# Performance work log

Measured on AMD Instinct MI355X. Metric: run time of the kernel, lower is better.

The kernel has to match this reference:

```python
import jax, jax.numpy as jnp
import numpy as np

H = 8            # heads
SCALE = (512 // H) ** -0.5  # dim_head^-0.5
EPS = 1e-5


def ln(x, w, b):
    mu = jnp.mean(x, axis=-1, keepdims=True)
    var = jnp.var(x, axis=-1, keepdims=True)
    return (x - mu) / jnp.sqrt(var + EPS) * w + b


def attention(x, ctx, wq, wkv, wo, bo):
    # x: [b, i, d], ctx: [b, j, d_ctx]
    b, i, _ = x.shape
    q = x @ wq                       # [b, i, h*dh]
    k, v = jnp.split(ctx @ wkv, 2, axis=-1)
    split_heads = lambda t: t.reshape(t.shape[0], t.shape[1], H, -1).transpose(0, 2, 1, 3)
    q, k, v = split_heads(q), split_heads(k), split_heads(v)
    sim = jnp.einsum('bhid,bhjd->bhij', q, k) * SCALE
    attn = jax.nn.softmax(sim, axis=-1)
    out = jnp.einsum('bhij,bhjd->bhid', attn, v)
    out = out.transpose(0, 2, 1, 3).reshape(b, i, -1)
    return out @ wo + bo


def geglu_ff(x, w1, b1, w2, b2):
    h = x @ w1 + b1
    a, g = jnp.split(h, 2, axis=-1)
    return (a * jax.nn.gelu(g, approximate=False)) @ w2 + b2


def setup_inputs() -> dict:
    key = jax.random.key(0)
    ks = jax.random.split(key, 12)
    D, FF, B, L, N = 512, 2048, 8, 128, 4096
    r = lambda k, s: jax.random.normal(k, s, jnp.float32) * 0.02
    return {
        'context': jax.random.normal(ks[0], (B, N, D), jnp.float32),
        'latents': jax.random.normal(ks[1], (B, L, D), jnp.float32),
        'ca_ln_w': jnp.ones((D,), jnp.float32), 'ca_ln_b': jnp.zeros((D,), jnp.float32),
        'ca_lnc_w': jnp.ones((D,), jnp.float32), 'ca_lnc_b': jnp.zeros((D,), jnp.float32),
        'ca_wq': r(ks[2], (D, D)), 'ca_wkv': r(ks[3], (D, 2 * D)),
        'ca_wo': r(ks[4], (D, D)), 'ca_bo': jnp.zeros((D,), jnp.float32),
        'cf_ln_w': jnp.ones((D,), jnp.float32), 'cf_ln_b': jnp.zeros((D,), jnp.float32),
        'cf_w1': r(ks[5], (D, 2 * FF)), 'cf_b1': jnp.zeros((2 * FF,), jnp.float32),
        'cf_w2': r(ks[6], (FF, D)), 'cf_b2': jnp.zeros((D,), jnp.float32),
        'sa_ln_w': jnp.ones((D,), jnp.float32), 'sa_ln_b': jnp.zeros((D,), jnp.float32),
        'sa_wq': r(ks[7], (D, D)), 'sa_wkv': r(ks[8], (D, 2 * D)),
        'sa_wo': r(ks[9], (D, D)), 'sa_bo': jnp.zeros((D,), jnp.float32),
        'lf_ln_w': jnp.ones((D,), jnp.float32), 'lf_ln_b': jnp.zeros((D,), jnp.float32),
        'lf_w1': r(ks[10], (D, 2 * FF)), 'lf_b1': jnp.zeros((2 * FF,), jnp.float32),
        'lf_w2': r(ks[11], (FF, D)), 'lf_b2': jnp.zeros((D,), jnp.float32),
    }


def reference(context, latents,
              ca_ln_w, ca_ln_b, ca_lnc_w, ca_lnc_b, ca_wq, ca_wkv, ca_wo, ca_bo,
              cf_ln_w, cf_ln_b, cf_w1, cf_b1, cf_w2, cf_b2,
              sa_ln_w, sa_ln_b, sa_wq, sa_wkv, sa_wo, sa_bo,
              lf_ln_w, lf_ln_b, lf_w1, lf_b1, lf_w2, lf_b2):
    x = latents
    # PreNorm cross-attention (with context LayerNorm) + residual
    xn = ln(x, ca_ln_w, ca_ln_b)
    cn = ln(context, ca_lnc_w, ca_lnc_b)
    x = attention(xn, cn, ca_wq, ca_wkv, ca_wo, ca_bo) + x
    # PreNorm cross FFN (GEGLU) + residual
    x = geglu_ff(ln(x, cf_ln_w, cf_ln_b), cf_w1, cf_b1, cf_w2, cf_b2) + x
    # PreNorm latent self-attention + residual
    xn = ln(x, sa_ln_w, sa_ln_b)
    x = attention(xn, xn, sa_wq, sa_wkv, sa_wo, sa_bo) + x
    # PreNorm latent FFN (GEGLU) + residual
    x = geglu_ff(ln(x, lf_ln_w, lf_ln_b), lf_w1, lf_b1, lf_w2, lf_b2) + x
    return x
```

## Files before the change

kernel.cpp:

```cpp
#include <hip/hip_runtime.h>
#include <hip/hip_bf16.h>
#include <math.h>


typedef __attribute__((ext_vector_type(8))) short bf16x8;
typedef __attribute__((ext_vector_type(4))) float f32x4;
typedef long i64;
typedef __attribute__((ext_vector_type(2))) long i64x2;

#define DEVI __device__ __forceinline__

DEVI void load_lds16(const void* g, void* l) {
  __builtin_amdgcn_global_load_lds(
      (const __attribute__((address_space(1))) void*)g,
      (__attribute__((address_space(3))) void*)l, 16, 0, 0);
}

DEVI short bfbits(float x) {
  __hip_bfloat16 h = __float2bfloat16(x);
  return *reinterpret_cast<short*>(&h);
}

DEVI unsigned int fp8pk2(float a, float b) {
  return __builtin_amdgcn_cvt_pk_fp8_f32(a, b, 0, false) & 0xffff;
}

DEVI unsigned char fp8b(float x) {
  return (unsigned char)(__builtin_amdgcn_cvt_pk_fp8_f32(x, x, 0, false) & 0xff);
}

__global__ __launch_bounds__(256, 4) void gemm_sk(
    const __hip_bfloat16* __restrict__ A, const __hip_bfloat16* __restrict__ Bt,
    float* __restrict__ P, int M, int N, int K) {
  const int nwg = gridDim.x * gridDim.y;
  const int lid = blockIdx.y * gridDim.x + blockIdx.x;
  const int work = (lid & 7) * (nwg >> 3) + (lid >> 3);
  const int n0 = (work % gridDim.x) * 128;
  const int m0 = (work / gridDim.x) * 128;
  const int KS = K / gridDim.z;
  const int kbeg = blockIdx.z * KS;

  const int t = threadIdx.x;
  const int w = t >> 6, l = t & 63;
  const int lr = l & 15, lk = l >> 4;
  const int wm = (w >> 1) * 64, wn = (w & 1) * 64;
  __shared__ __hip_bfloat16 Al[2][128 * 32];
  __shared__ __hip_bfloat16 Bl[2][128 * 32];

  f32x4 acc[4][4];
  const f32x4 z = {0.f, 0.f, 0.f, 0.f};
#pragma unroll
  for (int i = 0; i < 4; ++i)
#pragma unroll
    for (int j = 0; j < 4; ++j) acc[i][j] = z;

  const int srow = w * 16 + (l >> 2);
  const int scol = ((l & 3) ^ ((l >> 3) & 3)) * 8;
  const __hip_bfloat16* Ag = A + (size_t)(m0 + srow) * K + kbeg + scol;
  const __hip_bfloat16* Bg = Bt + (size_t)(n0 + srow) * K + kbeg + scol;

#define STAGE(buf, k0)                                                   \
  {                                                                      \
    load_lds16(Ag + (k0), (char*)Al[buf] + w * 1024);                    \
    load_lds16(Ag + (size_t)64 * K + (k0), (char*)Al[buf] + 4096 + w * 1024); \
    load_lds16(Bg + (k0), (char*)Bl[buf] + w * 1024);                    \
    load_lds16(Bg + (size_t)64 * K + (k0), (char*)Bl[buf] + 4096 + w * 1024); \
  }

  STAGE(0, 0);
  __syncthreads();
  int cur = 0;
  const int rs = (lk ^ ((lr >> 1) & 3)) * 16;
  for (int k0 = 0; k0 < KS; k0 += 32) {
    if (k0 + 32 < KS) STAGE(cur ^ 1, k0 + 32);
    bf16x8 af[4], bfr[4];
#pragma unroll
    for (int i = 0; i < 4; ++i)
      af[i] = *(const bf16x8*)((const char*)Al[cur] + ((wm + i * 16 + lr) * 64 + rs));
#pragma unroll
    for (int j = 0; j < 4; ++j)
      bfr[j] = *(const bf16x8*)((const char*)Bl[cur] + ((wn + j * 16 + lr) * 64 + rs));
#pragma unroll
    for (int i = 0; i < 4; ++i)
#pragma unroll
      for (int j = 0; j < 4; ++j)
        acc[i][j] = __builtin_amdgcn_mfma_f32_16x16x32_bf16(af[i], bfr[j], acc[i][j], 0, 0, 0);
    __syncthreads();
    cur ^= 1;
  }
#undef STAGE

  float* Pz = P + (size_t)blockIdx.z * M * N;
#pragma unroll
  for (int i = 0; i < 4; ++i) {
    const int row = m0 + wm + i * 16 + lk * 4;
#pragma unroll
    for (int j = 0; j < 4; ++j) {
      const int col = n0 + wn + j * 16 + lr;
#pragma unroll
      for (int r = 0; r < 4; ++r)
        Pz[(size_t)(row + r) * N + col] = acc[i][j][r];
    }
  }
}

__global__ __launch_bounds__(256) void reduce_sk(
    const float* __restrict__ P, const float* __restrict__ bias,
    const float* __restrict__ res, float* __restrict__ out, int SK) {
  const int i = (blockIdx.x * 256 + threadIdx.x) * 4;
  f32x4 v = *(const f32x4*)&bias[i & 511];
  const f32x4 rr = *(const f32x4*)&res[i];
  v += rr;
  for (int s = 0; s < SK; ++s) v += *(const f32x4*)&P[(size_t)s * 524288 + i];
  *(f32x4*)&out[i] = v;
}

__global__ __launch_bounds__(256) void reduce_ln_sk(
    const float* __restrict__ P, const float* __restrict__ bias,
    const float* __restrict__ res, float* __restrict__ xout,
    const float* __restrict__ w, const float* __restrict__ b,
    __hip_bfloat16* __restrict__ y, int SK) {
  const int row = blockIdx.x * 4 + (threadIdx.x >> 6);
  const int l = threadIdx.x & 63;
  const size_t base = (size_t)row * 512 + l * 8;
  f32x4 v0 = *(const f32x4*)&res[base];
  f32x4 v1 = *(const f32x4*)&res[base + 4];
  v0 += *(const f32x4*)&bias[l * 8];
  v1 += *(const f32x4*)&bias[l * 8 + 4];
  for (int s = 0; s < SK; ++s) {
    v0 += *(const f32x4*)&P[(size_t)s * 524288 + base];
    v1 += *(const f32x4*)&P[(size_t)s * 524288 + base + 4];
  }
  *(f32x4*)&xout[base] = v0;
  *(f32x4*)&xout[base + 4] = v1;
  float s1 = 0.f, s2 = 0.f;
#pragma unroll
  for (int e = 0; e < 4; ++e) {
    s1 += v0[e] + v1[e];
    s2 += v0[e] * v0[e] + v1[e] * v1[e];
  }
#pragma unroll
  for (int d = 1; d < 64; d <<= 1) {
    s1 += __shfl_xor(s1, d);
    s2 += __shfl_xor(s2, d);
  }
  const float mean = s1 * (1.f / 512.f);
  const float var = s2 * (1.f / 512.f) - mean * mean;
  const float rstd = rsqrtf(var + 1e-5f);
  const f32x4 w0 = *(const f32x4*)&w[l * 8], w1 = *(const f32x4*)&w[l * 8 + 4];
  const f32x4 b0 = *(const f32x4*)&b[l * 8], b1 = *(const f32x4*)&b[l * 8 + 4];
  bf16x8 o;
#pragma unroll
  for (int e = 0; e < 4; ++e) {
    o[e] = bfbits((v0[e] - mean) * rstd * w0[e] + b0[e]);
    o[e + 4] = bfbits((v1[e] - mean) * rstd * w1[e] + b1[e]);
  }
  *(bf16x8*)&y[base] = o;
}

__global__ __launch_bounds__(256, 4) void gemm_geglu(
    const __hip_bfloat16* __restrict__ A, const __hip_bfloat16* __restrict__ Bt,
    __hip_bfloat16* __restrict__ Cb, const float* __restrict__ bias) {
  const int K = 512;
  const int nwg = gridDim.x * gridDim.y;
  const int lid = blockIdx.y * gridDim.x + blockIdx.x;
  const int work = (lid & 7) * (nwg >> 3) + (lid >> 3);
  const int n0 = (work % gridDim.x) * 128;
  const int m0 = (work / gridDim.x) * 64;

  const int t = threadIdx.x;
  const int w = t >> 6, l = t & 63;
  const int lr = l & 15, lk = l >> 4;
  const int wm = (w >> 1) * 32, wn = (w & 1) * 64;
  __shared__ __hip_bfloat16 Al[2][64 * 32];
  __shared__ __hip_bfloat16 Bl[2][128 * 32];

  f32x4 acc[2][4];
  const f32x4 z = {0.f, 0.f, 0.f, 0.f};
#pragma unroll
  for (int i = 0; i < 2; ++i)
#pragma unroll
    for (int j = 0; j < 4; ++j) acc[i][j] = z;

  const int srow = w * 16 + (l >> 2);
  const int scol = ((l & 3) ^ ((l >> 3) & 3)) * 8;
  const __hip_bfloat16* Ag = A + (size_t)(m0 + srow) * K + scol;
  const __hip_bfloat16* Bg = Bt + (size_t)(n0 + srow) * K + scol;

#define STAGE(buf, k0)                                                   \
  {                                                                      \
    load_lds16(Ag + (k0), (char*)Al[buf] + w * 1024);                    \
    load_lds16(Bg + (k0), (char*)Bl[buf] + w * 1024);                    \
    load_lds16(Bg + (size_t)64 * K + (k0), (char*)Bl[buf] + 4096 + w * 1024); \
  }

  STAGE(0, 0);
  __syncthreads();
  int cur = 0;
  const int rs = (lk ^ ((lr >> 1) & 3)) * 16;
  for (int k0 = 0; k0 < K; k0 += 32) {
    if (k0 + 32 < K) STAGE(cur ^ 1, k0 + 32);
    bf16x8 af[2], bfr[4];
#pragma unroll
    for (int i = 0; i < 2; ++i)
      af[i] = *(const bf16x8*)((const char*)Al[cur] + ((wm + i * 16 + lr) * 64 + rs));
#pragma unroll
    for (int j = 0; j < 4; ++j)
      bfr[j] = *(const bf16x8*)((const char*)Bl[cur] + ((wn + j * 16 + lr) * 64 + rs));
#pragma unroll
    for (int i = 0; i < 2; ++i)
#pragma unroll
      for (int j = 0; j < 4; ++j)
        acc[i][j] = __builtin_amdgcn_mfma_f32_16x16x32_bf16(af[i], bfr[j], acc[i][j], 0, 0, 0);
    __syncthreads();
    cur ^= 1;
  }
#undef STAGE

  const int nb = (n0 + wn) >> 1;
  float ba[2], bg[2];
#pragma unroll
  for (int jj = 0; jj < 2; ++jj) {
    ba[jj] = bias[nb + jj * 16 + lr];
    bg[jj] = bias[2048 + nb + jj * 16 + lr];
  }
#pragma unroll
  for (int i = 0; i < 2; ++i) {
    const int row = m0 + wm + i * 16 + lk * 4;
#pragma unroll
    for (int jj = 0; jj < 2; ++jj) {
      const int col = nb + jj * 16 + lr;
#pragma unroll
      for (int r = 0; r < 4; ++r) {
        const float a = acc[i][jj][r] + ba[jj];
        const float g = acc[i][jj + 2][r] + bg[jj];
        const float ge = 0.5f * g * (1.f + erff(g * 0.70710678118f));
        Cb[(size_t)(row + r) * 2048 + col] = __float2bfloat16(a * ge);
      }
    }
  }
}

__global__ __launch_bounds__(256, 4) void projx_kernel(
    const unsigned char* __restrict__ ctx8, const unsigned char* __restrict__ wkv8,
    __hip_bfloat16* __restrict__ Kb, __hip_bfloat16* __restrict__ Vt,
    const unsigned char* __restrict__ xq8, const unsigned char* __restrict__ wq8,
    __hip_bfloat16* __restrict__ Qb) {
  const int nwg = gridDim.x;
  const int lid = blockIdx.x;
  const int work = (lid & 7) * (nwg >> 3) + (lid >> 3);

  const unsigned char *A, *Bt;
  int m0, n0, mode;
  if (work < 2048) {
    m0 = (work >> 3) * 128;
    n0 = (work & 7) * 128;
    A = ctx8; Bt = wkv8;
    mode = (n0 < 512) ? 0 : 1;
  } else {
    const int idx = work - 2048;
    m0 = (idx >> 2) * 128;
    n0 = (idx & 3) * 128;
    A = xq8; Bt = wq8;
    mode = 2;
  }

  const int t = threadIdx.x;
  const int w = t >> 6, l = t & 63;
  const int lr = l & 15, lk = l >> 4;
  const int wm = (w >> 1) * 64, wn = (w & 1) * 64;
  __shared__ unsigned char Al[2][128 * 64];
  __shared__ unsigned char Bl[2][128 * 64];

  f32x4 acc[4][4];
  const f32x4 z = {0.f, 0.f, 0.f, 0.f};
#pragma unroll
  for (int i = 0; i < 4; ++i)
#pragma unroll
    for (int j = 0; j < 4; ++j) acc[i][j] = z;

  const int srow = w * 16 + (l >> 2);
  const int sc = ((l & 3) ^ ((l >> 3) & 3)) * 16;
  const unsigned char* Ag = A + (size_t)(m0 + srow) * 512 + sc;
  const unsigned char* Bg = Bt + (size_t)(n0 + srow) * 512 + sc;

#define STAGE(buf, kb)                                                   \
  {                                                                      \
    load_lds16(Ag + (kb), (char*)Al[buf] + w * 1024);                    \
    load_lds16(Ag + (size_t)64 * 512 + (kb), (char*)Al[buf] + 4096 + w * 1024); \
    load_lds16(Bg + (kb), (char*)Bl[buf] + w * 1024);                    \
    load_lds16(Bg + (size_t)64 * 512 + (kb), (char*)Bl[buf] + 4096 + w * 1024); \
  }

  STAGE(0, 0);
  __syncthreads();
  int cur = 0;
  const int rs = (lk ^ ((lr >> 1) & 3)) * 16;
  for (int tt = 0; tt < 8; ++tt) {
    if (tt < 7) STAGE(cur ^ 1, (tt + 1) * 64);
    i64 af[2][4], bfr[2][4];
#pragma unroll
    for (int i = 0; i < 4; ++i) {
      const int ar = wm + i * 16 + lr;
      const i64x2 v = *(const i64x2*)((const char*)Al[cur] + ar * 64 + rs);
      af[0][i] = v[0];
      af[1][i] = v[1];
    }
#pragma unroll
    for (int j = 0; j < 4; ++j) {
      const int br = wn + j * 16 + lr;
      const i64x2 v = *(const i64x2*)((const char*)Bl[cur] + br * 64 + rs);
      bfr[0][j] = v[0];
      bfr[1][j] = v[1];
    }
#pragma unroll
    for (int i = 0; i < 4; ++i)
#pragma unroll
      for (int j = 0; j < 4; ++j) {
        acc[i][j] = __builtin_amdgcn_mfma_f32_16x16x32_fp8_fp8(af[0][i], bfr[0][j], acc[i][j], 0, 0, 0);
        acc[i][j] = __builtin_amdgcn_mfma_f32_16x16x32_fp8_fp8(af[1][i], bfr[1][j], acc[i][j], 0, 0, 0);
      }
    __syncthreads();
    cur ^= 1;
  }
#undef STAGE

  const float SCL = 0.0625f;
  if (mode == 0) {
#pragma unroll
    for (int i = 0; i < 4; ++i) {
      const int row = m0 + wm + i * 16 + lk * 4;
#pragma unroll
      for (int j = 0; j < 4; ++j) {
        const int col = n0 + wn + j * 16 + lr;
#pragma unroll
        for (int r = 0; r < 4; ++r)
          Kb[(size_t)(row + r) * 512 + col] = __float2bfloat16(acc[i][j][r] * SCL);
      }
    }
  } else if (mode == 1) {
#pragma unroll
    for (int i = 0; i < 4; ++i) {
      const int row0 = m0 + wm + i * 16 + lk * 4;
      const int b = row0 >> 12;
      const int key0 = row0 & 4095;
#pragma unroll
      for (int j = 0; j < 4; ++j) {
        const int c = n0 + wn + j * 16 + lr - 512;
        const int hh = c >> 6, dh = c & 63;
        short4 pk;
        pk.x = bfbits(acc[i][j][0] * SCL);
        pk.y = bfbits(acc[i][j][1] * SCL);
        pk.z = bfbits(acc[i][j][2] * SCL);
        pk.w = bfbits(acc[i][j][3] * SCL);
        *(short4*)&Vt[((size_t)((b * 8 + hh) * 64 + dh) << 12) + key0] = pk;
      }
    }
  } else {
#pragma unroll
    for (int i = 0; i < 4; ++i) {
      const int row = m0 + wm + i * 16 + lk * 4;
#pragma unroll
      for (int j = 0; j < 4; ++j) {
        const int col = n0 + wn + j * 16 + lr;
#pragma unroll
        for (int r = 0; r < 4; ++r)
          Qb[(size_t)(row + r) * 512 + col] = __float2bfloat16(acc[i][j][r] * SCL);
      }
    }
  }
}

__global__ __launch_bounds__(256, 4) void proj_kernel(
    const __hip_bfloat16* __restrict__ A, const __hip_bfloat16* __restrict__ Bt,
    __hip_bfloat16* __restrict__ Qb, __hip_bfloat16* __restrict__ Kb,
    __hip_bfloat16* __restrict__ Vt, int qcols, int rpb_shift) {
  const int nwg = gridDim.x * gridDim.y;
  const int lid = blockIdx.y * gridDim.x + blockIdx.x;
  const int work = (lid & 7) * (nwg >> 3) + (lid >> 3);
  const int n0 = (work % gridDim.x) * 128;
  const int m0 = (work / gridDim.x) * 128;
  const int K = 512;

  const int t = threadIdx.x;
  const int w = t >> 6, l = t & 63;
  const int lr = l & 15, lk = l >> 4;
  const int wm = (w >> 1) * 64, wn = (w & 1) * 64;
  __shared__ __hip_bfloat16 Al[2][128 * 32];
  __shared__ __hip_bfloat16 Bl[2][128 * 32];

  f32x4 acc[4][4];
  const f32x4 z = {0.f, 0.f, 0.f, 0.f};
#pragma unroll
  for (int i = 0; i < 4; ++i)
#pragma unroll
    for (int j = 0; j < 4; ++j) acc[i][j] = z;

  const int srow = w * 16 + (l >> 2);
  const int scol = ((l & 3) ^ ((l >> 3) & 3)) * 8;
  const __hip_bfloat16* Ag = A + (size_t)(m0 + srow) * K + scol;
  const __hip_bfloat16* Bg = Bt + (size_t)(n0 + srow) * K + scol;

#define STAGE(buf, k0)                                                   \
  {                                                                      \
    load_lds16(Ag + (k0), (char*)Al[buf] + w * 1024);                    \
    load_lds16(Ag + (size_t)64 * K + (k0), (char*)Al[buf] + 4096 + w * 1024); \
    load_lds16(Bg + (k0), (char*)Bl[buf] + w * 1024);                    \
    load_lds16(Bg + (size_t)64 * K + (k0), (char*)Bl[buf] + 4096 + w * 1024); \
  }

  STAGE(0, 0);
  __syncthreads();
  int cur = 0;
  const int rs = (lk ^ ((lr >> 1) & 3)) * 16;
  for (int k0 = 0; k0 < K; k0 += 32) {
    if (k0 + 32 < K) STAGE(cur ^ 1, k0 + 32);
    bf16x8 af[4], bfr[4];
#pragma unroll
    for (int i = 0; i < 4; ++i)
      af[i] = *(const bf16x8*)((const char*)Al[cur] + ((wm + i * 16 + lr) * 64 + rs));
#pragma unroll
    for (int j = 0; j < 4; ++j)
      bfr[j] = *(const bf16x8*)((const char*)Bl[cur] + ((wn + j * 16 + lr) * 64 + rs));
#pragma unroll
    for (int i = 0; i < 4; ++i)
#pragma unroll
      for (int j = 0; j < 4; ++j)
        acc[i][j] = __builtin_amdgcn_mfma_f32_16x16x32_bf16(af[i], bfr[j], acc[i][j], 0, 0, 0);
    __syncthreads();
    cur ^= 1;
  }
#undef STAGE

  if (n0 < qcols) {
#pragma unroll
    for (int i = 0; i < 4; ++i) {
      const int row = m0 + wm + i * 16 + lk * 4;
#pragma unroll
      for (int j = 0; j < 4; ++j) {
        const int col = n0 + wn + j * 16 + lr;
#pragma unroll
        for (int r = 0; r < 4; ++r)
          Qb[(size_t)(row + r) * 512 + col] = __float2bfloat16(acc[i][j][r]);
      }
    }
  } else if (n0 < qcols + 512) {
#pragma unroll
    for (int i = 0; i < 4; ++i) {
      const int row = m0 + wm + i * 16 + lk * 4;
#pragma unroll
      for (int j = 0; j < 4; ++j) {
        const int col = n0 + wn + j * 16 + lr - qcols;
#pragma unroll
        for (int r = 0; r < 4; ++r)
          Kb[(size_t)(row + r) * 512 + col] = __float2bfloat16(acc[i][j][r]);
      }
    }
  } else {
    const int rpb = 1 << rpb_shift;
#pragma unroll
    for (int i = 0; i < 4; ++i) {
      const int row0 = m0 + wm + i * 16 + lk * 4;
      const int b = row0 >> rpb_shift;
      const int key0 = row0 & (rpb - 1);
#pragma unroll
      for (int j = 0; j < 4; ++j) {
        const int c = n0 + wn + j * 16 + lr - qcols - 512;
        const int hh = c >> 6, dh = c & 63;
        short4 pk;
        pk.x = bfbits(acc[i][j][0]);
        pk.y = bfbits(acc[i][j][1]);
        pk.z = bfbits(acc[i][j][2]);
        pk.w = bfbits(acc[i][j][3]);
        *(short4*)&Vt[((size_t)((b * 8 + hh) * 64 + dh) << rpb_shift) + key0] = pk;
      }
    }
  }
}

__global__ __launch_bounds__(256) void attn_split_kernel(
    const __hip_bfloat16* __restrict__ Q, const __hip_bfloat16* __restrict__ Kb,
    const __hip_bfloat16* __restrict__ Vt,
    __hip_bfloat16* __restrict__ Opart, float* __restrict__ Lv,
    __hip_bfloat16* __restrict__ Od,
    int chunk, int rows_per_b, int S) {
  const float SC2 = 0.18033688f;
  const int h = blockIdx.x, b = blockIdx.y, s = blockIdx.z;
  const int t = threadIdx.x;
  const int w = t >> 6, l = t & 63;
  const int lr = l & 15, lk = l >> 4;
  __shared__ __hip_bfloat16 Kl[64 * 64];
  __shared__ __hip_bfloat16 Vl[64 * 64];
  __shared__ __hip_bfloat16 Pl[4][32 * 64];

  bf16x8 qf[2][2];
#pragma unroll
  for (int mf = 0; mf < 2; ++mf)
#pragma unroll
    for (int kf = 0; kf < 2; ++kf)
      qf[mf][kf] = *(const bf16x8*)&Q[(size_t)(b * 128 + w * 32 + mf * 16 + lr) * 512 +
                                      h * 64 + kf * 32 + lk * 8];

  f32x4 o[2][4];
  const f32x4 z = {0.f, 0.f, 0.f, 0.f};
#pragma unroll
  for (int mf = 0; mf < 2; ++mf)
#pragma unroll
    for (int nf = 0; nf < 4; ++nf) o[mf][nf] = z;
  float lsum[2][4];
#pragma unroll
  for (int mf = 0; mf < 2; ++mf)
#pragma unroll
    for (int r = 0; r < 4; ++r) lsum[mf][r] = 0.f;

  const __hip_bfloat16* kvb = Kb + (size_t)b * rows_per_b * 512;
  const __hip_bfloat16* vtb = Vt + (size_t)(b * 8 + h) * 64 * rows_per_b;
  char* pw = (char*)Pl[w];
  const int srow = l >> 3;
  const int sslot = (l & 7) ^ srow;
  const int jend = s * chunk + chunk;

  for (int j0 = s * chunk; j0 < jend; j0 += 64) {
    __syncthreads();
#pragma unroll
    for (int p = 0; p < 2; ++p) {
      const int row = p * 32 + w * 8 + srow;
      load_lds16(&kvb[(size_t)(j0 + row) * 512 + h * 64 + sslot * 8],
                 (char*)Kl + p * 4096 + w * 1024);
      load_lds16(&vtb[(size_t)row * rows_per_b + j0 + sslot * 8],
                 (char*)Vl + p * 4096 + w * 1024);
    }
    __syncthreads();

    f32x4 sc[2][4];
#pragma unroll
    for (int mf = 0; mf < 2; ++mf)
#pragma unroll
      for (int nf = 0; nf < 4; ++nf) sc[mf][nf] = z;
    __builtin_amdgcn_s_setprio(1);
#pragma unroll
    for (int kf = 0; kf < 2; ++kf) {
      bf16x8 kb[4];
#pragma unroll
      for (int nf = 0; nf < 4; ++nf) {
        const int key = nf * 16 + lr;
        kb[nf] = *(const bf16x8*)((char*)Kl +
                  (key * 128 + (((kf * 4 + lk) ^ (key & 7)) * 16)));
      }
#pragma unroll
      for (int mf = 0; mf < 2; ++mf)
#pragma unroll
        for (int nf = 0; nf < 4; ++nf)
          sc[mf][nf] = __builtin_amdgcn_mfma_f32_16x16x32_bf16(qf[mf][kf], kb[nf], sc[mf][nf], 0, 0, 0);
    }
    __builtin_amdgcn_s_setprio(0);

#pragma unroll
    for (int mf = 0; mf < 2; ++mf)
#pragma unroll
      for (int nf = 0; nf < 4; ++nf)
#pragma unroll
        for (int r = 0; r < 4; ++r) {
          const float p = exp2f(sc[mf][nf][r] * SC2);
          sc[mf][nf][r] = p;
          lsum[mf][r] += p;
        }

#pragma unroll
    for (int mf = 0; mf < 2; ++mf)
#pragma unroll
      for (int r = 0; r < 4; ++r) {
        const int prow = mf * 16 + lk * 4 + r;
#pragma unroll
        for (int nf = 0; nf < 4; ++nf) {
          const int pcol = nf * 16 + lr;
          *(__hip_bfloat16*)(pw + ((prow * 128 + pcol * 2) ^ ((prow & 7) << 4))) =
              __float2bfloat16(sc[mf][nf][r]);
        }
      }

    __builtin_amdgcn_s_setprio(1);
#pragma unroll
    for (int kf = 0; kf < 2; ++kf) {
      bf16x8 pa[2], vb[4];
#pragma unroll
      for (int mf = 0; mf < 2; ++mf) {
        const int prow = mf * 16 + lr;
        pa[mf] = *(const bf16x8*)(pw + ((prow * 128 + (kf * 4 + lk) * 16) ^ ((prow & 7) << 4)));
      }
#pragma unroll
      for (int nf = 0; nf < 4; ++nf) {
        const int dh = nf * 16 + lr;
        vb[nf] = *(const bf16x8*)((char*)Vl +
                  (dh * 128 + (((kf * 4 + lk) ^ (dh & 7)) * 16)));
      }
#pragma unroll
      for (int mf = 0; mf < 2; ++mf)
#pragma unroll
        for (int nf = 0; nf < 4; ++nf)
          o[mf][nf] = __builtin_amdgcn_mfma_f32_16x16x32_bf16(pa[mf], vb[nf], o[mf][nf], 0, 0, 0);
    }
    __builtin_amdgcn_s_setprio(0);
  }

  const int part = (b * 8 + h) * S + s;
  __hip_bfloat16* op = Opart + (size_t)part * 8192;
#pragma unroll
  for (int mf = 0; mf < 2; ++mf)
#pragma unroll
    for (int r = 0; r < 4; ++r) {
      float ls = lsum[mf][r];
      ls += __shfl_xor(ls, 1);
      ls += __shfl_xor(ls, 2);
      ls += __shfl_xor(ls, 4);
      ls += __shfl_xor(ls, 8);
      const int row = w * 32 + mf * 16 + lk * 4 + r;
      if (Od) {
        const float inv = 1.f / ls;
#pragma unroll
        for (int nf = 0; nf < 4; ++nf)
          Od[(size_t)(b * 128 + row) * 512 + h * 64 + nf * 16 + lr] =
              __float2bfloat16(o[mf][nf][r] * inv);
      } else {
#pragma unroll
        for (int nf = 0; nf < 4; ++nf)
          op[(size_t)row * 64 + nf * 16 + lr] = __float2bfloat16(o[mf][nf][r]);
        if (lr == 0) Lv[(size_t)part * 128 + row] = ls;
      }
    }
}

__global__ __launch_bounds__(256) void attn_combine_kernel(
    const __hip_bfloat16* __restrict__ Opart, const float* __restrict__ Lv,
    __hip_bfloat16* __restrict__ O, int S) {
  const int row = blockIdx.x;
  const int b = row >> 7, i = row & 127;
  const int t = threadIdx.x;
  const int h = t >> 5, dh0 = (t * 2) & 63;
  const int pbase = (b * 8 + h) * S;
  float L = 0.f, v0 = 0.f, v1 = 0.f;
  for (int s = 0; s < S; ++s) {
    L += Lv[(size_t)(pbase + s) * 128 + i];
    const __hip_bfloat16* p = &Opart[((size_t)(pbase + s) * 128 + i) * 64 + dh0];
    const ushort2 u = *(const ushort2*)p;
    const unsigned int b0 = (unsigned int)u.x << 16, b1 = (unsigned int)u.y << 16;
    v0 += *(const float*)&b0;
    v1 += *(const float*)&b1;
  }
  const float inv = 1.f / L;
  ushort2 out;
  out.x = (unsigned short)bfbits(v0 * inv);
  out.y = (unsigned short)bfbits(v1 * inv);
  *(ushort2*)&O[(size_t)row * 512 + t * 2] = out;
}

DEVI void ln_wave_q(const float* __restrict__ x, const float* __restrict__ w,
                    const float* __restrict__ bb, unsigned char* __restrict__ y,
                    int row) {
  const int l = threadIdx.x & 63;
  const size_t base = (size_t)row * 512 + l * 8;
  const f32x4 v0 = *(const f32x4*)&x[base];
  const f32x4 v1 = *(const f32x4*)&x[base + 4];
  float s = 0.f, sq = 0.f;
#pragma unroll
  for (int e = 0; e < 4; ++e) {
    s += v0[e] + v1[e];
    sq += v0[e] * v0[e] + v1[e] * v1[e];
  }
#pragma unroll
  for (int d = 1; d < 64; d <<= 1) {
    s += __shfl_xor(s, d);
    sq += __shfl_xor(sq, d);
  }
  const float mean = s * (1.f / 512.f);
  const float var = sq * (1.f / 512.f) - mean * mean;
  const float rstd = rsqrtf(var + 1e-5f);
  const f32x4 w0 = *(const f32x4*)&w[l * 8], w1 = *(const f32x4*)&w[l * 8 + 4];
  const f32x4 b0 = *(const f32x4*)&bb[l * 8], b1 = *(const f32x4*)&bb[l * 8 + 4];
  float yv[8];
#pragma unroll
  for (int e = 0; e < 4; ++e) {
    yv[e] = (v0[e] - mean) * rstd * w0[e] + b0[e];
    yv[e + 4] = (v1[e] - mean) * rstd * w1[e] + b1[e];
  }
  uint2 pk;
  pk.x = fp8pk2(yv[0], yv[1]) | (fp8pk2(yv[2], yv[3]) << 16);
  pk.y = fp8pk2(yv[4], yv[5]) | (fp8pk2(yv[6], yv[7]) << 16);
  const int gg = l & 7;
  const size_t wb = (size_t)row * 512 + (l >> 3) * 64 +
                    ((gg & 3) * 2 + (gg >> 2)) * 8;
  *(uint2*)&y[wb] = pk;
}

struct WcvtDesc { const float* src[10]; __hip_bfloat16* dst[10]; };

__global__ __launch_bounds__(256) void prep_kernel(
    WcvtDesc d, unsigned char* __restrict__ wq8, unsigned char* __restrict__ wkv8,
    const float* __restrict__ lat, const float* __restrict__ lw,
    const float* __restrict__ lb, unsigned char* __restrict__ xq8,
    const float* __restrict__ ctx, const float* __restrict__ cw,
    const float* __restrict__ cb, unsigned char* __restrict__ cn8) {
  if (blockIdx.x >= 8192) {
    const int row = (blockIdx.x - 8192) * 4 + (threadIdx.x >> 6);
    if (row < 1024)
      ln_wave_q(lat, lw, lb, xq8, row);
    else
      ln_wave_q(ctx, cw, cb, cn8, row - 1024);
    return;
  }
  int tile = blockIdx.x;
  const int set = tile >> 12;
  tile &= 4095;
  int wi0, K, N, base;
  if (tile < 256)       { wi0 = 0; K = 512;  N = 512;  base = 0; }
  else if (tile < 768)  { wi0 = 1; K = 512;  N = 1024; base = 256; }
  else if (tile < 1024) { wi0 = 2; K = 512;  N = 512;  base = 768; }
  else if (tile < 3072) { wi0 = 3; K = 512;  N = 4096; base = 1024; }
  else                  { wi0 = 4; K = 2048; N = 512;  base = 3072; }
  const bool permute = (wi0 == 3);
  const bool tofp8 = (set == 0 && wi0 < 2);
  const int wi = wi0 + set * 5;
  const int rel = tile - base;
  const int ntx = N >> 5;
  const int n0 = (rel % ntx) * 32, k0 = (rel / ntx) * 32;
  const int sn0 = permute ? (((n0 >> 6) << 5) + ((n0 & 32) ? 2048 : 0)) : n0;
  const float* W = d.src[wi];
  __shared__ float tl[32][33];
  const int tx = threadIdx.x & 31, ty = threadIdx.x >> 5;
#pragma unroll
  for (int j = 0; j < 4; ++j)
    tl[ty + j * 8][tx] = W[(size_t)(k0 + ty + j * 8) * N + sn0 + tx];
  __syncthreads();
  if (tofp8) {
    unsigned char* Wq = (wi0 == 0) ? wq8 : wkv8;
    const int k = k0 + tx;
    const int gg = (k >> 3) & 7;
    const int kp = (k & ~63) + ((gg & 3) * 2 + (gg >> 2)) * 8 + (k & 7);
#pragma unroll
    for (int j = 0; j < 4; ++j)
      Wq[(size_t)(n0 + ty + j * 8) * 512 + kp] = fp8b(tl[tx][ty + j * 8] * 16.f);
  } else {
    __hip_bfloat16* Wt = d.dst[wi];
#pragma unroll
    for (int j = 0; j < 4; ++j)
      Wt[(size_t)(n0 + ty + j * 8) * K + k0 + tx] = __float2bfloat16(tl[tx][ty + j * 8]);
  }
}

extern "C" void kernel_launch(void* const* d_in, const int* in_sizes, int n_in,
                              void* d_out, int out_size, void* d_ws, size_t ws_size,
                              hipStream_t stream) {
  (void)in_sizes; (void)n_in; (void)out_size; (void)ws_size;
  const float* context = (const float*)d_in[0];
  const float* latents = (const float*)d_in[1];
  const float* ca_ln_w = (const float*)d_in[2];
  const float* ca_ln_b = (const float*)d_in[3];
  const float* ca_lnc_w = (const float*)d_in[4];
  const float* ca_lnc_b = (const float*)d_in[5];
  const float* ca_wq = (const float*)d_in[6];
  const float* ca_wkv = (const float*)d_in[7];
  const float* ca_wo = (const float*)d_in[8];
  const float* ca_bo = (const float*)d_in[9];
  const float* cf_ln_w = (const float*)d_in[10];
  const float* cf_ln_b = (const float*)d_in[11];
  const float* cf_w1 = (const float*)d_in[12];
  const float* cf_b1 = (const float*)d_in[13];
  const float* cf_w2 = (const float*)d_in[14];
  const float* cf_b2 = (const float*)d_in[15];
  const float* sa_ln_w = (const float*)d_in[16];
  const float* sa_ln_b = (const float*)d_in[17];
  const float* sa_wq = (const float*)d_in[18];
  const float* sa_wkv = (const float*)d_in[19];
  const float* sa_wo = (const float*)d_in[20];
  const float* sa_bo = (const float*)d_in[21];
  const float* lf_ln_w = (const float*)d_in[22];
  const float* lf_ln_b = (const float*)d_in[23];
  const float* lf_w1 = (const float*)d_in[24];
  const float* lf_b1 = (const float*)d_in[25];
  const float* lf_w2 = (const float*)d_in[26];
  const float* lf_b2 = (const float*)d_in[27];

  typedef __hip_bfloat16 bf;
  char* ws = (char*)d_ws;
  size_t off = 0;
  auto alloc = [&](size_t bytes) -> void* {
    void* p = ws + off;
    off += (bytes + 255) & ~(size_t)255;
    return p;
  };
  bf* wq1t = (bf*)alloc((size_t)512 * 512 * 2);
  bf* wkv1t = (bf*)alloc((size_t)1024 * 512 * 2);
  bf* wo1t = (bf*)alloc((size_t)512 * 512 * 2);
  bf* w1ct = (bf*)alloc((size_t)4096 * 512 * 2);
  bf* w2ct = (bf*)alloc((size_t)512 * 2048 * 2);
  bf* wq2t = (bf*)alloc((size_t)512 * 512 * 2);
  bf* wkv2t = (bf*)alloc((size_t)1024 * 512 * 2);
  bf* wo2t = (bf*)alloc((size_t)512 * 512 * 2);
  bf* w1lt = (bf*)alloc((size_t)4096 * 512 * 2);
  bf* w2lt = (bf*)alloc((size_t)512 * 2048 * 2);
  unsigned char* wq8 = (unsigned char*)alloc((size_t)512 * 512);
  unsigned char* wkv8 = (unsigned char*)alloc((size_t)1024 * 512);
  unsigned char* cn8 = (unsigned char*)alloc((size_t)32768 * 512);
  unsigned char* xq8 = (unsigned char*)alloc((size_t)1024 * 512);
  bf* cn = (bf*)alloc((size_t)32768 * 512 * 2);
  bf* kbuf = (bf*)alloc((size_t)32768 * 512 * 2);
  bf* vt = (bf*)alloc((size_t)64 * 64 * 4096 * 2);
  bf* kb2 = (bf*)alloc((size_t)1024 * 512 * 2);
  bf* vt2 = (bf*)alloc((size_t)64 * 64 * 128 * 2);
  float* lv = (float*)alloc((size_t)1024 * 128 * 4);
  float* skq = (float*)alloc((size_t)4 * 1024 * 512 * 4);
  bf* xnb = (bf*)alloc((size_t)1024 * 512 * 2);
  bf* qb = (bf*)alloc((size_t)1024 * 512 * 2);
  bf* aob = (bf*)alloc((size_t)1024 * 512 * 2);
  bf* q2b = (bf*)alloc((size_t)1024 * 512 * 2);
  bf* ao2b = (bf*)alloc((size_t)1024 * 512 * 2);
  float* x1 = (float*)alloc((size_t)1024 * 512 * 4);
  float* x2 = (float*)alloc((size_t)1024 * 512 * 4);
  float* x3 = (float*)alloc((size_t)1024 * 512 * 4);
  bf* x2n = (bf*)alloc((size_t)1024 * 512 * 2);
  bf* x3n = (bf*)alloc((size_t)1024 * 512 * 2);
  bf* opart = cn;
  float* skp = (float*)cn;
  bf* agb = (bf*)((char*)cn + 17 * 1024 * 1024);

  WcvtDesc wd;
  wd.src[0] = ca_wq;  wd.dst[0] = wq1t;
  wd.src[1] = ca_wkv; wd.dst[1] = wkv1t;
  wd.src[2] = ca_wo;  wd.dst[2] = wo1t;
  wd.src[3] = cf_w1;  wd.dst[3] = w1ct;
  wd.src[4] = cf_w2;  wd.dst[4] = w2ct;
  wd.src[5] = sa_wq;  wd.dst[5] = wq2t;
  wd.src[6] = sa_wkv; wd.dst[6] = wkv2t;
  wd.src[7] = sa_wo;  wd.dst[7] = wo2t;
  wd.src[8] = lf_w1;  wd.dst[8] = w1lt;
  wd.src[9] = lf_w2;  wd.dst[9] = w2lt;

  prep_kernel<<<8192 + 8448, 256, 0, stream>>>(
      wd, wq8, wkv8, latents, ca_ln_w, ca_ln_b, xq8,
      context, ca_lnc_w, ca_lnc_b, cn8);

  projx_kernel<<<2080, 256, 0, stream>>>(cn8, wkv8, kbuf, vt, xq8, wq8, qb);
  attn_split_kernel<<<dim3(8, 8, 16), 256, 0, stream>>>(qb, kbuf, vt, opart, lv, nullptr, 256, 4096, 16);
  attn_combine_kernel<<<1024, 256, 0, stream>>>(opart, lv, aob, 16);
  gemm_sk<<<dim3(4, 8, 4), 256, 0, stream>>>(aob, wo1t, skq, 1024, 512, 512);
  reduce_ln_sk<<<256, 256, 0, stream>>>(skq, ca_bo, latents, x1, cf_ln_w, cf_ln_b, xnb, 4);

  gemm_geglu<<<dim3(32, 16), 256, 0, stream>>>(xnb, w1ct, agb, cf_b1);
  gemm_sk<<<dim3(4, 8, 8), 256, 0, stream>>>(agb, w2ct, skp, 1024, 512, 2048);
  reduce_ln_sk<<<256, 256, 0, stream>>>(skp, cf_b2, x1, x2, sa_ln_w, sa_ln_b, x2n, 8);

  proj_kernel<<<dim3(12, 8), 256, 0, stream>>>(x2n, wq2t, q2b, kb2, vt2, 512, 7);
  attn_split_kernel<<<dim3(8, 8, 1), 256, 0, stream>>>(q2b, kb2, vt2, nullptr, nullptr, ao2b, 128, 128, 1);
  gemm_sk<<<dim3(4, 8, 4), 256, 0, stream>>>(ao2b, wo2t, skq, 1024, 512, 512);
  reduce_ln_sk<<<256, 256, 0, stream>>>(skq, sa_bo, x2, x3, lf_ln_w, lf_ln_b, x3n, 4);

  gemm_geglu<<<dim3(32, 16), 256, 0, stream>>>(x3n, w1lt, agb, lf_b1);
  gemm_sk<<<dim3(4, 8, 8), 256, 0, stream>>>(agb, w2lt, skp, 1024, 512, 2048);
  reduce_sk<<<512, 256, 0, stream>>>(skp, lf_b2, x3, (float*)d_out, 8);
}
```

Before: 191.4 us.

## Store cross-attention Q and K in FP8 and use FP8 MFMA for scores

The context projection now writes K and Q as FP8 bytes (scaled by 4, with a permuted column layout matching the FP8 MFMA operand order) instead of bf16. The cross-attention kernel is templated so the large cross-attention pass loads half as many K bytes into LDS with an XOR swizzle and computes QK^T with fp8 MFMA, while the latent self-attention keeps the bf16 path. This halves K write and read traffic over the 32k-row context and shrinks LDS use, at the cost of lower precision in the attention logits.

```diff
diff --git a/kernel.cpp b/kernel.cpp
--- a/kernel.cpp
+++ b/kernel.cpp
@@ -27,6 +27,11 @@
 
 DEVI unsigned char fp8b(float x) {
   return (unsigned char)(__builtin_amdgcn_cvt_pk_fp8_f32(x, x, 0, false) & 0xff);
+}
+
+DEVI int gpos(int col) {
+  const int g = (col >> 3) & 7;
+  return (col & ~63) + (g & 3) * 16 + (g >> 2) * 8 + (col & 7);
 }
 
 __global__ __launch_bounds__(256, 4) void gemm_sk(
@@ -243,9 +248,9 @@
 
 __global__ __launch_bounds__(256, 4) void projx_kernel(
     const unsigned char* __restrict__ ctx8, const unsigned char* __restrict__ wkv8,
-    __hip_bfloat16* __restrict__ Kb, __hip_bfloat16* __restrict__ Vt,
+    unsigned char* __restrict__ K8, __hip_bfloat16* __restrict__ Vt,
     const unsigned char* __restrict__ xq8, const unsigned char* __restrict__ wq8,
-    __hip_bfloat16* __restrict__ Qb) {
+    unsigned char* __restrict__ Q8) {
   const int nwg = gridDim.x;
   const int lid = blockIdx.x;
   const int work = (lid & 7) * (nwg >> 3) + (lid >> 3);
@@ -326,16 +331,17 @@
 #undef STAGE
 
   const float SCL = 0.0625f;
+  const float SQK = SCL * 4.f;
   if (mode == 0) {
 #pragma unroll
     for (int i = 0; i < 4; ++i) {
       const int row = m0 + wm + i * 16 + lk * 4;
 #pragma unroll
       for (int j = 0; j < 4; ++j) {
-        const int col = n0 + wn + j * 16 + lr;
+        const int bp = gpos(n0 + wn + j * 16 + lr);
 #pragma unroll
         for (int r = 0; r < 4; ++r)
-          Kb[(size_t)(row + r) * 512 + col] = __float2bfloat16(acc[i][j][r] * SCL);
+          K8[(size_t)(row + r) * 512 + bp] = fp8b(acc[i][j][r] * SQK);
       }
     }
   } else if (mode == 1) {
@@ -362,10 +368,10 @@
       const int row = m0 + wm + i * 16 + lk * 4;
 #pragma unroll
       for (int j = 0; j < 4; ++j) {
-        const int col = n0 + wn + j * 16 + lr;
+        const int bp = gpos(n0 + wn + j * 16 + lr);
 #pragma unroll
         for (int r = 0; r < 4; ++r)
-          Qb[(size_t)(row + r) * 512 + col] = __float2bfloat16(acc[i][j][r] * SCL);
+          Q8[(size_t)(row + r) * 512 + bp] = fp8b(acc[i][j][r] * SQK);
       }
     }
   }
@@ -478,28 +484,42 @@
   }
 }
 
+template <int QK8>
 __global__ __launch_bounds__(256) void attn_split_kernel(
-    const __hip_bfloat16* __restrict__ Q, const __hip_bfloat16* __restrict__ Kb,
+    const void* __restrict__ Qp, const void* __restrict__ Kp,
     const __hip_bfloat16* __restrict__ Vt,
     __hip_bfloat16* __restrict__ Opart, float* __restrict__ Lv,
     __hip_bfloat16* __restrict__ Od,
     int chunk, int rows_per_b, int S) {
-  const float SC2 = 0.18033688f;
+  const float SC2 = QK8 ? (0.18033688f / 16.f) : 0.18033688f;
   const int h = blockIdx.x, b = blockIdx.y, s = blockIdx.z;
   const int t = threadIdx.x;
   const int w = t >> 6, l = t & 63;
   const int lr = l & 15, lk = l >> 4;
-  __shared__ __hip_bfloat16 Kl[64 * 64];
+  __shared__ unsigned char Kraw[QK8 ? 4096 : 8192];
   __shared__ __hip_bfloat16 Vl[64 * 64];
   __shared__ __hip_bfloat16 Pl[4][32 * 64];
 
   bf16x8 qf[2][2];
-#pragma unroll
-  for (int mf = 0; mf < 2; ++mf)
-#pragma unroll
-    for (int kf = 0; kf < 2; ++kf)
-      qf[mf][kf] = *(const bf16x8*)&Q[(size_t)(b * 128 + w * 32 + mf * 16 + lr) * 512 +
-                                      h * 64 + kf * 32 + lk * 8];
+  i64 qf8[2][2];
+  if constexpr (QK8) {
+    const unsigned char* q8 = (const unsigned char*)Qp;
+#pragma unroll
+    for (int mf = 0; mf < 2; ++mf) {
+      const i64x2 qv = *(const i64x2*)&q8[(size_t)(b * 128 + w * 32 + mf * 16 + lr) * 512 +
+                                          h * 64 + lk * 16];
+      qf8[mf][0] = qv[0];
+      qf8[mf][1] = qv[1];
+    }
+  } else {
+    const __hip_bfloat16* Q = (const __hip_bfloat16*)Qp;
+#pragma unroll
+    for (int mf = 0; mf < 2; ++mf)
+#pragma unroll
+      for (int kf = 0; kf < 2; ++kf)
+        qf[mf][kf] = *(const bf16x8*)&Q[(size_t)(b * 128 + w * 32 + mf * 16 + lr) * 512 +
+                                        h * 64 + kf * 32 + lk * 8];
+  }
 
   f32x4 o[2][4];
   const f32x4 z = {0.f, 0.f, 0.f, 0.f};
@@ -513,7 +533,6 @@
 #pragma unroll
     for (int r = 0; r < 4; ++r) lsum[mf][r] = 0.f;
 
-  const __hip_bfloat16* kvb = Kb + (size_t)b * rows_per_b * 512;
   const __hip_bfloat16* vtb = Vt + (size_t)(b * 8 + h) * 64 * rows_per_b;
   char* pw = (char*)Pl[w];
   const int srow = l >> 3;
@@ -522,13 +541,27 @@
 
   for (int j0 = s * chunk; j0 < jend; j0 += 64) {
     __syncthreads();
-#pragma unroll
-    for (int p = 0; p < 2; ++p) {
-      const int row = p * 32 + w * 8 + srow;
-      load_lds16(&kvb[(size_t)(j0 + row) * 512 + h * 64 + sslot * 8],
-                 (char*)Kl + p * 4096 + w * 1024);
-      load_lds16(&vtb[(size_t)row * rows_per_b + j0 + sslot * 8],
-                 (char*)Vl + p * 4096 + w * 1024);
+    if constexpr (QK8) {
+      const unsigned char* k8b = (const unsigned char*)Kp + (size_t)b * rows_per_b * 512;
+      const int kr = t >> 2, kslot = t & 3;
+      const int src = kslot ^ ((kr >> 1) & 3);
+      load_lds16(&k8b[(size_t)(j0 + kr) * 512 + h * 64 + src * 16], (char*)Kraw + t * 16);
+#pragma unroll
+      for (int p = 0; p < 2; ++p) {
+        const int row = p * 32 + w * 8 + srow;
+        load_lds16(&vtb[(size_t)row * rows_per_b + j0 + sslot * 8],
+                   (char*)Vl + p * 4096 + w * 1024);
+      }
+    } else {
+      const __hip_bfloat16* kvb = (const __hip_bfloat16*)Kp + (size_t)b * rows_per_b * 512;
+#pragma unroll
+      for (int p = 0; p < 2; ++p) {
+        const int row = p * 32 + w * 8 + srow;
+        load_lds16(&kvb[(size_t)(j0 + row) * 512 + h * 64 + sslot * 8],
+                   (char*)Kraw + p * 4096 + w * 1024);
+        load_lds16(&vtb[(size_t)row * rows_per_b + j0 + sslot * 8],
+                   (char*)Vl + p * 4096 + w * 1024);
+      }
     }
     __syncthreads();
 
@@ -538,20 +571,34 @@
 #pragma unroll
       for (int nf = 0; nf < 4; ++nf) sc[mf][nf] = z;
     __builtin_amdgcn_s_setprio(1);
-#pragma unroll
-    for (int kf = 0; kf < 2; ++kf) {
-      bf16x8 kb[4];
+    if constexpr (QK8) {
+      const int rs8 = (lk ^ ((lr >> 1) & 3)) * 16;
 #pragma unroll
       for (int nf = 0; nf < 4; ++nf) {
         const int key = nf * 16 + lr;
-        kb[nf] = *(const bf16x8*)((char*)Kl +
-                  (key * 128 + (((kf * 4 + lk) ^ (key & 7)) * 16)));
-      }
-#pragma unroll
-      for (int mf = 0; mf < 2; ++mf)
-#pragma unroll
-        for (int nf = 0; nf < 4; ++nf)
-          sc[mf][nf] = __builtin_amdgcn_mfma_f32_16x16x32_bf16(qf[mf][kf], kb[nf], sc[mf][nf], 0, 0, 0);
+        const i64x2 kv = *(const i64x2*)((const char*)Kraw + key * 64 + rs8);
+#pragma unroll
+        for (int mf = 0; mf < 2; ++mf) {
+          sc[mf][nf] = __builtin_amdgcn_mfma_f32_16x16x32_fp8_fp8(qf8[mf][0], kv[0], sc[mf][nf], 0, 0, 0);
+          sc[mf][nf] = __builtin_amdgcn_mfma_f32_16x16x32_fp8_fp8(qf8[mf][1], kv[1], sc[mf][nf], 0, 0, 0);
+        }
+      }
+    } else {
+#pragma unroll
+      for (int kf = 0; kf < 2; ++kf) {
+        bf16x8 kb[4];
+#pragma unroll
+        for (int nf = 0; nf < 4; ++nf) {
+          const int key = nf * 16 + lr;
+          kb[nf] = *(const bf16x8*)((const char*)Kraw +
+                    (key * 128 + (((kf * 4 + lk) ^ (key & 7)) * 16)));
+        }
+#pragma unroll
+        for (int mf = 0; mf < 2; ++mf)
+#pragma unroll
+          for (int nf = 0; nf < 4; ++nf)
+            sc[mf][nf] = __builtin_amdgcn_mfma_f32_16x16x32_bf16(qf[mf][kf], kb[nf], sc[mf][nf], 0, 0, 0);
+      }
     }
     __builtin_amdgcn_s_setprio(0);
 
@@ -802,15 +849,15 @@
   unsigned char* wkv8 = (unsigned char*)alloc((size_t)1024 * 512);
   unsigned char* cn8 = (unsigned char*)alloc((size_t)32768 * 512);
   unsigned char* xq8 = (unsigned char*)alloc((size_t)1024 * 512);
+  unsigned char* k8 = (unsigned char*)alloc((size_t)32768 * 512);
+  unsigned char* q8 = (unsigned char*)alloc((size_t)1024 * 512);
   bf* cn = (bf*)alloc((size_t)32768 * 512 * 2);
-  bf* kbuf = (bf*)alloc((size_t)32768 * 512 * 2);
   bf* vt = (bf*)alloc((size_t)64 * 64 * 4096 * 2);
   bf* kb2 = (bf*)alloc((size_t)1024 * 512 * 2);
   bf* vt2 = (bf*)alloc((size_t)64 * 64 * 128 * 2);
   float* lv = (float*)alloc((size_t)1024 * 128 * 4);
   float* skq = (float*)alloc((size_t)4 * 1024 * 512 * 4);
   bf* xnb = (bf*)alloc((size_t)1024 * 512 * 2);
-  bf* qb = (bf*)alloc((size_t)1024 * 512 * 2);
   bf* aob = (bf*)alloc((size_t)1024 * 512 * 2);
   bf* q2b = (bf*)alloc((size_t)1024 * 512 * 2);
   bf* ao2b = (bf*)alloc((size_t)1024 * 512 * 2);
@@ -839,8 +886,8 @@
       wd, wq8, wkv8, latents, ca_ln_w, ca_ln_b, xq8,
       context, ca_lnc_w, ca_lnc_b, cn8);
 
-  projx_kernel<<<2080, 256, 0, stream>>>(cn8, wkv8, kbuf, vt, xq8, wq8, qb);
-  attn_split_kernel<<<dim3(8, 8, 16), 256, 0, stream>>>(qb, kbuf, vt, opart, lv, nullptr, 256, 4096, 16);
+  projx_kernel<<<2080, 256, 0, stream>>>(cn8, wkv8, k8, vt, xq8, wq8, q8);
+  attn_split_kernel<1><<<dim3(8, 8, 16), 256, 0, stream>>>(q8, k8, vt, opart, lv, nullptr, 256, 4096, 16);
   attn_combine_kernel<<<1024, 256, 0, stream>>>(opart, lv, aob, 16);
   gemm_sk<<<dim3(4, 8, 4), 256, 0, stream>>>(aob, wo1t, skq, 1024, 512, 512);
   reduce_ln_sk<<<256, 256, 0, stream>>>(skq, ca_bo, latents, x1, cf_ln_w, cf_ln_b, xnb, 4);
@@ -850,7 +897,7 @@
   reduce_ln_sk<<<256, 256, 0, stream>>>(skp, cf_b2, x1, x2, sa_ln_w, sa_ln_b, x2n, 8);
 
   proj_kernel<<<dim3(12, 8), 256, 0, stream>>>(x2n, wq2t, q2b, kb2, vt2, 512, 7);
-  attn_split_kernel<<<dim3(8, 8, 1), 256, 0, stream>>>(q2b, kb2, vt2, nullptr, nullptr, ao2b, 128, 128, 1);
+  attn_split_kernel<0><<<dim3(8, 8, 1), 256, 0, stream>>>(q2b, kb2, vt2, nullptr, nullptr, ao2b, 128, 128, 1);
   gemm_sk<<<dim3(4, 8, 4), 256, 0, stream>>>(ao2b, wo2t, skq, 1024, 512, 512);
   reduce_ln_sk<<<256, 256, 0, stream>>>(skq, sa_bo, x2, x3, lf_ln_w, lf_ln_b, x3n, 4);
 
```

New measurement: 187.9 us. No clear change (-1.8%).
